# Kernel optimization log

Measured on AMD Instinct MI355X. Metric: run time of the kernel, lower is better.

Reference implementation:

```python
import jax, jax.numpy as jnp
import numpy as np

IN_C, HID_C, OUT_C = 6, 128, 6
B, H, W = 8, 256, 256


def _make_weight(key, oc, ic):
    return jax.random.normal(key, (oc, ic, 5), dtype=jnp.float32) / np.sqrt(ic * 5)


def setup_inputs() -> dict:
    key = jax.random.key(0)
    ks = jax.random.split(key, 5)
    x = jax.random.normal(ks[0], (B, IN_C, H, W), dtype=jnp.float32)
    return {
        "x": x,
        "w1": _make_weight(ks[1], HID_C, IN_C),
        "b1": jnp.zeros((HID_C,), jnp.float32),
        "w2": _make_weight(ks[2], HID_C, HID_C),
        "b2": jnp.zeros((HID_C,), jnp.float32),
        "w3": _make_weight(ks[3], HID_C, HID_C),
        "b3": jnp.zeros((HID_C,), jnp.float32),
        "w4": _make_weight(ks[4], OUT_C, HID_C),
        "b4": jnp.zeros((OUT_C,), jnp.float32),
    }


def cross_conv(x, w, b):
    # w: [oc, ic, 5] -> dense 3x3 kernel with 5-point cross stencil
    oc, ic, _ = w.shape
    k = jnp.zeros((oc, ic, 3, 3), dtype=w.dtype)
    k = k.at[:, :, 1, 1].set(w[:, :, 0])  # center
    k = k.at[:, :, 0, 1].set(w[:, :, 1])  # up
    k = k.at[:, :, 2, 1].set(w[:, :, 2])  # down
    k = k.at[:, :, 1, 0].set(w[:, :, 3])  # left
    k = k.at[:, :, 1, 2].set(w[:, :, 4])  # right
    y = jax.lax.conv_general_dilated(
        x, k, window_strides=(1, 1), padding="SAME",
        dimension_numbers=("NCHW", "OIHW", "NCHW"))
    return y + b[None, :, None, None]


def reference(x, w1, b1, w2, b2, w3, b3, w4, b4):
    h = jax.nn.relu(cross_conv(x, w1, b1))
    h = jax.nn.relu(cross_conv(h, w2, b2))
    h = jax.nn.relu(cross_conv(h, w3, b3))
    return cross_conv(h, w4, b4)
```

## Files before the change

### kernel.cpp

```cpp
#include <hip/hip_runtime.h>


#define BB   8
#define HH   256
#define WW   256

typedef _Float16 f16x8 __attribute__((ext_vector_type(8)));
typedef float    f32x4 __attribute__((ext_vector_type(4)));

__device__ _Float16 W1g[128 * 32];
__device__ _Float16 W2g[20 * 128 * 32];
__device__ _Float16 W3g[20 * 128 * 32];
__device__ _Float16 W4g[5 * 16 * 128];

__global__ void prep(const float* __restrict__ w1, const float* __restrict__ w2,
                     const float* __restrict__ w3, const float* __restrict__ w4)
{
    int idx = blockIdx.x * 256 + threadIdx.x;
    if (idx < 81920) {
        int icb = idx & 31, oc = (idx >> 5) & 127, ks = idx >> 12;
        int tap = ks >> 2, ic = (ks & 3) * 32 + icb;
        W2g[idx] = (_Float16)w2[(oc * 128 + ic) * 5 + tap];
    } else if (idx < 163840) {
        int k = idx - 81920;
        int icb = k & 31, oc = (k >> 5) & 127, ks = k >> 12;
        int tap = ks >> 2, ic = (ks & 3) * 32 + icb;
        W3g[k] = (_Float16)w3[(oc * 128 + ic) * 5 + tap];
    } else if (idx < 174080) {
        int k = idx - 163840;
        int t = k / 2048, oc = (k >> 7) & 15, ic = k & 127;
        W4g[k] = (_Float16)((oc < 6) ? w4[(oc * 128 + ic) * 5 + t] : 0.f);
    } else if (idx < 178176) {
        int k = idx - 174080;
        int kk = k & 31, oc = k >> 5;
        float v = 0.f;
        if (kk < 30) {
            int tap = (kk * 43) >> 8;
            int ic = kk - 6 * tap;
            v = w1[(oc * 6 + ic) * 5 + tap];
        }
        W1g[k] = (_Float16)v;
    }
}

template<int HALF, bool EDGE>
__device__ __forceinline__ void g1_stage(const float* __restrict__ xb,
                                         _Float16* __restrict__ Ap,
                                         int px, int gi0, int gj0)
{
#pragma unroll
    for (int it = 0; it < 15; ++it) {
        const int k = 2 * it + HALF;
        const int tap = k / 6, ic = k - 6 * tap;
        const int DI = (tap == 1) ? -1 : ((tap == 2) ? 1 : 0);
        const int DJ = (tap == 3) ? -1 : ((tap == 4) ? 1 : 0);
        const float* sp = xb + ic * 65536 + DI * 256 + DJ;
        float v;
        if (EDGE) {
            const int gi = gi0 + DI, gj = gj0 + DJ;
            v = ((unsigned)gi < 256u && (unsigned)gj < 256u) ? *sp : 0.f;
        } else {
            v = *sp;
        }
        Ap[px * 40 + k] = (_Float16)v;
    }
    Ap[px * 40 + 30 + HALF] = (_Float16)0.f;
}

__global__ __launch_bounds__(256, 3) void g1(
    const float* __restrict__ x, const float* __restrict__ bias,
    _Float16* __restrict__ outp)
{
    __shared__ _Float16 Ap[128 * 40];
    const int tid = threadIdx.x;
    const int j0 = blockIdx.x * 16, i0 = blockIdx.y * 8, b = blockIdx.z;
    const int px = tid & 127, half = tid >> 7;
    const int pr = px >> 4, pp = px & 15;
    const bool edge = (blockIdx.y == 0) | (blockIdx.y == 31) |
                      (blockIdx.x == 0) | (blockIdx.x == 15);
    const int gi0 = i0 + pr, gj0 = j0 + pp;
    const float* xb = x + (size_t)b * 6 * 65536 + gi0 * 256 + gj0;

    if (edge) {
        if (half == 0) g1_stage<0, true >(xb, Ap, px, gi0, gj0);
        else           g1_stage<1, true >(xb, Ap, px, gi0, gj0);
    } else {
        if (half == 0) g1_stage<0, false>(xb, Ap, px, gi0, gj0);
        else           g1_stage<1, false>(xb, Ap, px, gi0, gj0);
    }
    __syncthreads();

    const int lane = tid & 63, w = tid >> 6, l16 = lane & 15, quad = lane >> 4;
    f32x4 acc[2][8] = {};
    f16x8 a0 = *(const f16x8*)&Ap[((2 * w + 0) * 16 + l16) * 40 + quad * 8];
    f16x8 a1 = *(const f16x8*)&Ap[((2 * w + 1) * 16 + l16) * 40 + quad * 8];
#pragma unroll
    for (int nf = 0; nf < 8; ++nf) {
        f16x8 bf = *(const f16x8*)&W1g[(nf * 16 + l16) * 32 + quad * 8];
        acc[0][nf] = __builtin_amdgcn_mfma_f32_16x16x32_f16(a0, bf, acc[0][nf], 0, 0, 0);
        acc[1][nf] = __builtin_amdgcn_mfma_f32_16x16x32_f16(a1, bf, acc[1][nf], 0, 0, 0);
    }
#pragma unroll
    for (int mf = 0; mf < 2; ++mf) {
        const size_t rowb = ((size_t)b * 256 + i0 + 2 * w + mf) * 256 + j0;
#pragma unroll
        for (int nf = 0; nf < 8; ++nf) {
            const float bv = bias[nf * 16 + l16];
#pragma unroll
            for (int r = 0; r < 4; ++r)
                outp[(rowb + quad * 4 + r) * 128 + nf * 16 + l16] =
                    (_Float16)fmaxf(acc[mf][nf][r] + bv, 0.f);
        }
    }
}

template<int LAYER>
__global__ __launch_bounds__(256, 2) void gmid(
    const _Float16* __restrict__ in, const float* __restrict__ bias,
    _Float16* __restrict__ outp)
{
    const _Float16* wt = (LAYER == 2) ? W2g : W3g;
    __shared__ __align__(16) _Float16 Al[180 * 128];
    const int tid = threadIdx.x;
    const int lane = tid & 63, w = tid >> 6;
    const int j0 = blockIdx.x * 16, i0 = blockIdx.y * 8, b = blockIdx.z;
    const bool top = (blockIdx.y == 0), bot = (blockIdx.y == 31);
    const bool left = (blockIdx.x == 0), right = (blockIdx.x == 15);

    {
        const int pxl = lane & 15;
#pragma unroll
        for (int k = 0; k < 12; ++k) {
            const int m = w + 4 * k;
            if (m < 45) {
                const int s = 4 * m + (lane >> 4);
                const int r = (s * 114) >> 11;
                const int p = s - 18 * r;
                int gi = i0 - 1 + r; gi = gi < 0 ? 0 : (gi > 255 ? 255 : gi);
                int gj = j0 - 1 + p; gj = gj < 0 ? 0 : (gj > 255 ? 255 : gj);
                const _Float16* src = in + (((size_t)(b * 256 + gi)) * 256 + gj) * 128
                                         + ((pxl ^ (s & 7)) << 3);
                __builtin_amdgcn_global_load_lds(
                    (const __attribute__((address_space(1))) void*)src,
                    (__attribute__((address_space(3))) void*)(Al + m * 512),
                    16, 0, 0);
            }
        }
    }
    __syncthreads();
    if (top | bot | left | right) {
#pragma unroll
        for (int pass = 0; pass < 2; ++pass) {
            const int gidx = (tid >> 3) + 32 * pass, c = tid & 7;
            int sid = -1;
            if (gidx < 18)      { if (top)   sid = gidx; }
            else if (gidx < 36) { if (bot)   sid = 162 + gidx - 18; }
            else if (gidx < 46) { if (left)  sid = (gidx - 36) * 18; }
            else if (gidx < 56) { if (right) sid = (gidx - 46) * 18 + 17; }
            if (sid >= 0) {
                const f16x8 z = {};
                *(f16x8*)(Al + sid * 128 + c * 16)     = z;
                *(f16x8*)(Al + sid * 128 + c * 16 + 8) = z;
            }
        }
        __syncthreads();
    }

    const int l16 = lane & 15, quad = lane >> 4;
    const int n0 = w * 32;

    const _Float16* wb = wt + (size_t)(n0 + l16) * 32 + quad * 8;

    f32x4 acc[8][2] = {};
    const int DR[5] = {1, 0, 2, 1, 1}, DP[5] = {1, 1, 1, 0, 2};

    auto lda = [&](int ks, int r) -> f16x8 {
        const int tap = ks >> 2, kc = ks & 3;
        const int s = (DR[tap] + r) * 18 + DP[tap] + l16;
        const int ch = (kc * 4 + quad) ^ (s & 7);
        return *(const f16x8*)&Al[s * 128 + ch * 8];
    };

    f16x8 bc[2], bn[2], ac[8], an[8];
#pragma unroll
    for (int nf = 0; nf < 2; ++nf) bc[nf] = *(const f16x8*)(wb + nf * 512);
#pragma unroll
    for (int r = 0; r < 8; ++r) ac[r] = lda(0, r);

#pragma unroll
    for (int ks = 0; ks < 20; ++ks) {
        if (ks < 19) {
#pragma unroll
            for (int nf = 0; nf < 2; ++nf)
                bn[nf] = *(const f16x8*)(wb + (size_t)(ks + 1) * 4096 + nf * 512);
#pragma unroll
            for (int r = 0; r < 8; ++r) an[r] = lda(ks + 1, r);
        }
        __builtin_amdgcn_s_setprio(1);
#pragma unroll
        for (int r = 0; r < 8; ++r)
#pragma unroll
            for (int nf = 0; nf < 2; ++nf)
                acc[r][nf] = __builtin_amdgcn_mfma_f32_16x16x32_f16(
                    ac[r], bc[nf], acc[r][nf], 0, 0, 0);
        __builtin_amdgcn_s_setprio(0);
#pragma unroll
        for (int nf = 0; nf < 2; ++nf) bc[nf] = bn[nf];
#pragma unroll
        for (int r = 0; r < 8; ++r) ac[r] = an[r];
    }

#pragma unroll
    for (int r = 0; r < 8; ++r) {
        const size_t rowb = ((size_t)b * 256 + i0 + r) * 256 + j0;
#pragma unroll
        for (int nf = 0; nf < 2; ++nf) {
            const float bv = bias[n0 + nf * 16 + l16];
#pragma unroll
            for (int vi = 0; vi < 4; ++vi)
                outp[(rowb + quad * 4 + vi) * 128 + n0 + nf * 16 + l16] =
                    (_Float16)fmaxf(acc[r][nf][vi] + bv, 0.f);
        }
    }
}

__global__ __launch_bounds__(256, 3) void g4(
    const _Float16* __restrict__ in, const float* __restrict__ bias,
    float* __restrict__ outp)
{
    __shared__ __align__(16) _Float16 Al[180 * 128];
    const int tid = threadIdx.x;
    const int lane = tid & 63, w = tid >> 6;
    const int j0 = blockIdx.x * 16, i0 = blockIdx.y * 8, b = blockIdx.z;
    const bool top = (blockIdx.y == 0), bot = (blockIdx.y == 31);
    const bool left = (blockIdx.x == 0), right = (blockIdx.x == 15);

    {
        const int pxl = lane & 15;
#pragma unroll
        for (int k = 0; k < 12; ++k) {
            const int m = w + 4 * k;
            if (m < 45) {
                const int s = 4 * m + (lane >> 4);
                const int r = (s * 114) >> 11;
                const int p = s - 18 * r;
                int gi = i0 - 1 + r; gi = gi < 0 ? 0 : (gi > 255 ? 255 : gi);
                int gj = j0 - 1 + p; gj = gj < 0 ? 0 : (gj > 255 ? 255 : gj);
                const _Float16* src = in + (((size_t)(b * 256 + gi)) * 256 + gj) * 128
                                         + ((pxl ^ (s & 7)) << 3);
                __builtin_amdgcn_global_load_lds(
                    (const __attribute__((address_space(1))) void*)src,
                    (__attribute__((address_space(3))) void*)(Al + m * 512),
                    16, 0, 0);
            }
        }
    }
    __syncthreads();
    if (top | bot | left | right) {
#pragma unroll
        for (int pass = 0; pass < 2; ++pass) {
            const int gidx = (tid >> 3) + 32 * pass, c = tid & 7;
            int sid = -1;
            if (gidx < 18)      { if (top)   sid = gidx; }
            else if (gidx < 36) { if (bot)   sid = 162 + gidx - 18; }
            else if (gidx < 46) { if (left)  sid = (gidx - 36) * 18; }
            else if (gidx < 56) { if (right) sid = (gidx - 46) * 18 + 17; }
            if (sid >= 0) {
                const f16x8 z = {};
                *(f16x8*)(Al + sid * 128 + c * 16)     = z;
                *(f16x8*)(Al + sid * 128 + c * 16 + 8) = z;
            }
        }
        __syncthreads();
    }

    const int l16 = lane & 15, quad = lane >> 4;
    const int DR[5] = {1, 0, 2, 1, 1}, DP[5] = {1, 1, 1, 0, 2};

    auto lda = [&](int ks, int row) -> f16x8 {
        const int tap = ks >> 2, kc = ks & 3;
        const int s = (DR[tap] + row) * 18 + DP[tap] + l16;
        const int ch = (kc * 4 + quad) ^ (s & 7);
        return *(const f16x8*)&Al[s * 128 + ch * 8];
    };
    auto ldb = [&](int ks) -> f16x8 {
        const int tap = ks >> 2, kc = ks & 3;
        return *(const f16x8*)&W4g[(size_t)(tap * 16 + l16) * 128 + kc * 32 + quad * 8];
    };

    f32x4 acc[2] = {};
    f16x8 bfc = ldb(0), bfn;
    f16x8 afc0 = lda(0, 2 * w), afc1 = lda(0, 2 * w + 1), afn0, afn1;
#pragma unroll
    for (int ks = 0; ks < 20; ++ks) {
        if (ks < 19) {
            bfn  = ldb(ks + 1);
            afn0 = lda(ks + 1, 2 * w);
            afn1 = lda(ks + 1, 2 * w + 1);
        }
        __builtin_amdgcn_s_setprio(1);
        acc[0] = __builtin_amdgcn_mfma_f32_16x16x32_f16(afc0, bfc, acc[0], 0, 0, 0);
        acc[1] = __builtin_amdgcn_mfma_f32_16x16x32_f16(afc1, bfc, acc[1], 0, 0, 0);
        __builtin_amdgcn_s_setprio(0);
        bfc = bfn; afc0 = afn0; afc1 = afn1;
    }

    if (l16 < 6) {
        const float bb = bias[l16];
#pragma unroll
        for (int f = 0; f < 2; ++f) {
            const int i = i0 + 2 * w + f;
#pragma unroll
            for (int vi = 0; vi < 4; ++vi) {
                int jj = j0 + quad * 4 + vi;
                outp[(((size_t)b * 6 + l16) << 16) + i * 256 + jj] = acc[f][vi] + bb;
            }
        }
    }
}

extern "C" void kernel_launch(void* const* d_in, const int* in_sizes, int n_in,
                              void* d_out, int out_size, void* d_ws, size_t ws_size,
                              hipStream_t stream) {
    const float* x  = (const float*)d_in[0];
    const float* w1 = (const float*)d_in[1];
    const float* b1 = (const float*)d_in[2];
    const float* w2 = (const float*)d_in[3];
    const float* b2 = (const float*)d_in[4];
    const float* w3 = (const float*)d_in[5];
    const float* b3 = (const float*)d_in[6];
    const float* w4 = (const float*)d_in[7];
    const float* b4 = (const float*)d_in[8];
    float* out = (float*)d_out;

    const size_t act = (size_t)BB * HH * WW * 128;
    _Float16* A1 = (_Float16*)d_ws;
    _Float16* A2 = A1 + act;

    prep<<<696, 256, 0, stream>>>(w1, w2, w3, w4);
    dim3 blk(256, 1, 1);
    dim3 gm(16, 32, 8);
    g1<<<gm, blk, 0, stream>>>(x, b1, A1);
    gmid<2><<<gm, blk, 0, stream>>>(A1, b2, A2);
    gmid<3><<<gm, blk, 0, stream>>>(A2, b3, A1);
    g4<<<gm, blk, 0, stream>>>(A1, b4, out);
}
```

Before: 348.5 us.

## Make mid-layer conv blocks persistent over batch, prefetching next tile during stores

The two hidden-layer conv kernels now launch one block per spatial tile and loop over all 8 batch images inside the block. After the MFMA loop for one image finishes, the block issues the async global-to-LDS loads for the next image before writing the current outputs, so staging overlaps the store epilogue. Weight pointers and bias values are hoisted out of the loop. This cuts block scheduling and tail overhead, but adds intra-block barriers and leaves a single LDS buffer, so overlap is limited.

Measured after the change: 608.5 us. 74.6% more time.

```diff
diff --git a/kernel.cpp b/kernel.cpp
--- a/kernel.cpp
+++ b/kernel.cpp
@@ -123,6 +123,133 @@
     __shared__ __align__(16) _Float16 Al[180 * 128];
     const int tid = threadIdx.x;
     const int lane = tid & 63, w = tid >> 6;
+    const int j0 = blockIdx.x * 16, i0 = blockIdx.y * 8;
+    const bool top = (blockIdx.y == 0), bot = (blockIdx.y == 31);
+    const bool left = (blockIdx.x == 0), right = (blockIdx.x == 15);
+    const bool edge = top | bot | left | right;
+    const int pxl = lane & 15;
+
+    auto stage = [&](int bb) {
+#pragma unroll
+        for (int k = 0; k < 12; ++k) {
+            const int m = w + 4 * k;
+            if (m < 45) {
+                const int s = 4 * m + (lane >> 4);
+                const int r = (s * 114) >> 11;
+                const int p = s - 18 * r;
+                int gi = i0 - 1 + r; gi = gi < 0 ? 0 : (gi > 255 ? 255 : gi);
+                int gj = j0 - 1 + p; gj = gj < 0 ? 0 : (gj > 255 ? 255 : gj);
+                const _Float16* src = in + (((size_t)(bb * 256 + gi)) * 256 + gj) * 128
+                                         + ((pxl ^ (s & 7)) << 3);
+                __builtin_amdgcn_global_load_lds(
+                    (const __attribute__((address_space(1))) void*)src,
+                    (__attribute__((address_space(3))) void*)(Al + m * 512),
+                    16, 0, 0);
+            }
+        }
+    };
+
+    auto fixup = [&]() {
+#pragma unroll
+        for (int pass = 0; pass < 2; ++pass) {
+            const int gidx = (tid >> 3) + 32 * pass, c = tid & 7;
+            int sid = -1;
+            if (gidx < 18)      { if (top)   sid = gidx; }
+            else if (gidx < 36) { if (bot)   sid = 162 + gidx - 18; }
+            else if (gidx < 46) { if (left)  sid = (gidx - 36) * 18; }
+            else if (gidx < 56) { if (right) sid = (gidx - 46) * 18 + 17; }
+            if (sid >= 0) {
+                const f16x8 z = {};
+                *(f16x8*)(Al + sid * 128 + c * 16)     = z;
+                *(f16x8*)(Al + sid * 128 + c * 16 + 8) = z;
+            }
+        }
+    };
+
+    const int l16 = lane & 15, quad = lane >> 4;
+    const int n0 = w * 32;
+    const _Float16* wb = wt + (size_t)(n0 + l16) * 32 + quad * 8;
+    const int DR[5] = {1, 0, 2, 1, 1}, DP[5] = {1, 1, 1, 0, 2};
+    const float bv0 = bias[n0 + l16], bv1 = bias[n0 + 16 + l16];
+
+    auto lda = [&](int ks, int r) -> f16x8 {
+        const int tap = ks >> 2, kc = ks & 3;
+        const int s = (DR[tap] + r) * 18 + DP[tap] + l16;
+        const int ch = (kc * 4 + quad) ^ (s & 7);
+        return *(const f16x8*)&Al[s * 128 + ch * 8];
+    };
+
+    stage(0);
+    __syncthreads();
+    if (edge) { fixup(); __syncthreads(); }
+
+#pragma unroll 1
+    for (int t = 0; t < 8; ++t) {
+        f32x4 acc[8][2] = {};
+        f16x8 bc[2], bn[2], ac[8], an[8];
+#pragma unroll
+        for (int nf = 0; nf < 2; ++nf) bc[nf] = *(const f16x8*)(wb + nf * 512);
+#pragma unroll
+        for (int r = 0; r < 8; ++r) ac[r] = lda(0, r);
+
+#pragma unroll
+        for (int ks = 0; ks < 20; ++ks) {
+            if (ks < 19) {
+#pragma unroll
+                for (int nf = 0; nf < 2; ++nf)
+                    bn[nf] = *(const f16x8*)(wb + (size_t)(ks + 1) * 4096 + nf * 512);
+#pragma unroll
+                for (int r = 0; r < 8; ++r) an[r] = lda(ks + 1, r);
+            }
+            __builtin_amdgcn_s_setprio(1);
+#pragma unroll
+            for (int r = 0; r < 8; ++r)
+#pragma unroll
+                for (int nf = 0; nf < 2; ++nf)
+                    acc[r][nf] = __builtin_amdgcn_mfma_f32_16x16x32_f16(
+                        ac[r], bc[nf], acc[r][nf], 0, 0, 0);
+            __builtin_amdgcn_s_setprio(0);
+#pragma unroll
+            for (int nf = 0; nf < 2; ++nf) bc[nf] = bn[nf];
+#pragma unroll
+            for (int r = 0; r < 8; ++r) ac[r] = an[r];
+        }
+
+        if (t < 7) {
+            asm volatile("s_waitcnt lgkmcnt(0)" ::: "memory");
+            __builtin_amdgcn_sched_barrier(0);
+            __builtin_amdgcn_s_barrier();
+            stage(t + 1);
+        }
+
+#pragma unroll
+        for (int r = 0; r < 8; ++r) {
+            const size_t rowb = ((size_t)t * 256 + i0 + r) * 256 + j0;
+#pragma unroll
+            for (int vi = 0; vi < 4; ++vi) {
+                outp[(rowb + quad * 4 + vi) * 128 + n0 + l16] =
+                    (_Float16)fmaxf(acc[r][0][vi] + bv0, 0.f);
+                outp[(rowb + quad * 4 + vi) * 128 + n0 + 16 + l16] =
+                    (_Float16)fmaxf(acc[r][1][vi] + bv1, 0.f);
+            }
+        }
+
+        if (t < 7) {
+            asm volatile("s_waitcnt vmcnt(0)" ::: "memory");
+            __builtin_amdgcn_sched_barrier(0);
+            __builtin_amdgcn_s_barrier();
+            if (edge) { fixup(); __syncthreads(); }
+        }
+    }
+}
+
+__global__ __launch_bounds__(256, 3) void g4(
+    const _Float16* __restrict__ in, const float* __restrict__ bias,
+    float* __restrict__ outp)
+{
+    __shared__ __align__(16) _Float16 Al[180 * 128];
+    const int tid = threadIdx.x;
+    const int lane = tid & 63, w = tid >> 6;
     const int j0 = blockIdx.x * 16, i0 = blockIdx.y * 8, b = blockIdx.z;
     const bool top = (blockIdx.y == 0), bot = (blockIdx.y == 31);
     const bool left = (blockIdx.x == 0), right = (blockIdx.x == 15);
@@ -167,114 +294,6 @@
     }
 
     const int l16 = lane & 15, quad = lane >> 4;
-    const int n0 = w * 32;
-
-    const _Float16* wb = wt + (size_t)(n0 + l16) * 32 + quad * 8;
-
-    f32x4 acc[8][2] = {};
-    const int DR[5] = {1, 0, 2, 1, 1}, DP[5] = {1, 1, 1, 0, 2};
-
-    auto lda = [&](int ks, int r) -> f16x8 {
-        const int tap = ks >> 2, kc = ks & 3;
-        const int s = (DR[tap] + r) * 18 + DP[tap] + l16;
-        const int ch = (kc * 4 + quad) ^ (s & 7);
-        return *(const f16x8*)&Al[s * 128 + ch * 8];
-    };
-
-    f16x8 bc[2], bn[2], ac[8], an[8];
-#pragma unroll
-    for (int nf = 0; nf < 2; ++nf) bc[nf] = *(const f16x8*)(wb + nf * 512);
-#pragma unroll
-    for (int r = 0; r < 8; ++r) ac[r] = lda(0, r);
-
-#pragma unroll
-    for (int ks = 0; ks < 20; ++ks) {
-        if (ks < 19) {
-#pragma unroll
-            for (int nf = 0; nf < 2; ++nf)
-                bn[nf] = *(const f16x8*)(wb + (size_t)(ks + 1) * 4096 + nf * 512);
-#pragma unroll
-            for (int r = 0; r < 8; ++r) an[r] = lda(ks + 1, r);
-        }
-        __builtin_amdgcn_s_setprio(1);
-#pragma unroll
-        for (int r = 0; r < 8; ++r)
-#pragma unroll
-            for (int nf = 0; nf < 2; ++nf)
-                acc[r][nf] = __builtin_amdgcn_mfma_f32_16x16x32_f16(
-                    ac[r], bc[nf], acc[r][nf], 0, 0, 0);
-        __builtin_amdgcn_s_setprio(0);
-#pragma unroll
-        for (int nf = 0; nf < 2; ++nf) bc[nf] = bn[nf];
-#pragma unroll
-        for (int r = 0; r < 8; ++r) ac[r] = an[r];
-    }
-
-#pragma unroll
-    for (int r = 0; r < 8; ++r) {
-        const size_t rowb = ((size_t)b * 256 + i0 + r) * 256 + j0;
-#pragma unroll
-        for (int nf = 0; nf < 2; ++nf) {
-            const float bv = bias[n0 + nf * 16 + l16];
-#pragma unroll
-            for (int vi = 0; vi < 4; ++vi)
-                outp[(rowb + quad * 4 + vi) * 128 + n0 + nf * 16 + l16] =
-                    (_Float16)fmaxf(acc[r][nf][vi] + bv, 0.f);
-        }
-    }
-}
-
-__global__ __launch_bounds__(256, 3) void g4(
-    const _Float16* __restrict__ in, const float* __restrict__ bias,
-    float* __restrict__ outp)
-{
-    __shared__ __align__(16) _Float16 Al[180 * 128];
-    const int tid = threadIdx.x;
-    const int lane = tid & 63, w = tid >> 6;
-    const int j0 = blockIdx.x * 16, i0 = blockIdx.y * 8, b = blockIdx.z;
-    const bool top = (blockIdx.y == 0), bot = (blockIdx.y == 31);
-    const bool left = (blockIdx.x == 0), right = (blockIdx.x == 15);
-
-    {
-        const int pxl = lane & 15;
-#pragma unroll
-        for (int k = 0; k < 12; ++k) {
-            const int m = w + 4 * k;
-            if (m < 45) {
-                const int s = 4 * m + (lane >> 4);
-                const int r = (s * 114) >> 11;
-                const int p = s - 18 * r;
-                int gi = i0 - 1 + r; gi = gi < 0 ? 0 : (gi > 255 ? 255 : gi);
-                int gj = j0 - 1 + p; gj = gj < 0 ? 0 : (gj > 255 ? 255 : gj);
-                const _Float16* src = in + (((size_t)(b * 256 + gi)) * 256 + gj) * 128
-                                         + ((pxl ^ (s & 7)) << 3);
-                __builtin_amdgcn_global_load_lds(
-                    (const __attribute__((address_space(1))) void*)src,
-                    (__attribute__((address_space(3))) void*)(Al + m * 512),
-                    16, 0, 0);
-            }
-        }
-    }
-    __syncthreads();
-    if (top | bot | left | right) {
-#pragma unroll
-        for (int pass = 0; pass < 2; ++pass) {
-            const int gidx = (tid >> 3) + 32 * pass, c = tid & 7;
-            int sid = -1;
-            if (gidx < 18)      { if (top)   sid = gidx; }
-            else if (gidx < 36) { if (bot)   sid = 162 + gidx - 18; }
-            else if (gidx < 46) { if (left)  sid = (gidx - 36) * 18; }
-            else if (gidx < 56) { if (right) sid = (gidx - 46) * 18 + 17; }
-            if (sid >= 0) {
-                const f16x8 z = {};
-                *(f16x8*)(Al + sid * 128 + c * 16)     = z;
-                *(f16x8*)(Al + sid * 128 + c * 16 + 8) = z;
-            }
-        }
-        __syncthreads();
-    }
-
-    const int l16 = lane & 15, quad = lane >> 4;
     const int DR[5] = {1, 0, 2, 1, 1}, DP[5] = {1, 1, 1, 0, 2};
 
     auto lda = [&](int ks, int row) -> f16x8 {
@@ -341,7 +360,7 @@
     dim3 blk(256, 1, 1);
     dim3 gm(16, 32, 8);
     g1<<<gm, blk, 0, stream>>>(x, b1, A1);
-    gmid<2><<<gm, blk, 0, stream>>>(A1, b2, A2);
-    gmid<3><<<gm, blk, 0, stream>>>(A2, b3, A1);
+    gmid<2><<<dim3(16, 32, 1), blk, 0, stream>>>(A1, b2, A2);
+    gmid<3><<<dim3(16, 32, 1), blk, 0, stream>>>(A2, b3, A1);
     g4<<<gm, blk, 0, stream>>>(A1, b4, out);
 }
```

## Pre-convert input to NHWC fp16 and load layer-1 MFMA operands directly

Applied to the files above, without the earlier changes.

Adds a prepx kernel that transposes the fp32 NCHW input into an 8-channel-padded fp16 NHWC buffer, placed in the second activation workspace. Layer 1 then loads each tap's 8 channels as a single 16-byte vector straight into MFMA A fragments, doing two K=32 MFMAs per output tile. This replaces the shared-memory staging of 30 scalar strided loads and the block barrier. The cost is an extra kernel launch and a full pass over the input, plus padded work: the 5 taps are spread over 64 K slots instead of 30.

Result: no change. 354.6 us (+1.8%).

```diff
diff --git a/kernel.cpp b/kernel.cpp
--- a/kernel.cpp
+++ b/kernel.cpp
@@ -8,7 +8,7 @@
 typedef _Float16 f16x8 __attribute__((ext_vector_type(8)));
 typedef float    f32x4 __attribute__((ext_vector_type(4)));
 
-__device__ _Float16 W1g[128 * 32];
+__device__ _Float16 W1g2[128 * 64];
 __device__ _Float16 W2g[20 * 128 * 32];
 __device__ _Float16 W3g[20 * 128 * 32];
 __device__ _Float16 W4g[5 * 16 * 128];
@@ -30,76 +30,67 @@
         int k = idx - 163840;
         int t = k / 2048, oc = (k >> 7) & 15, ic = k & 127;
         W4g[k] = (_Float16)((oc < 6) ? w4[(oc * 128 + ic) * 5 + t] : 0.f);
-    } else if (idx < 178176) {
+    } else if (idx < 182272) {
         int k = idx - 174080;
-        int kk = k & 31, oc = k >> 5;
-        float v = 0.f;
-        if (kk < 30) {
-            int tap = (kk * 43) >> 8;
-            int ic = kk - 6 * tap;
-            v = w1[(oc * 6 + ic) * 5 + tap];
-        }
-        W1g[k] = (_Float16)v;
-    }
-}
-
-template<int HALF, bool EDGE>
-__device__ __forceinline__ void g1_stage(const float* __restrict__ xb,
-                                         _Float16* __restrict__ Ap,
-                                         int px, int gi0, int gj0)
-{
-#pragma unroll
-    for (int it = 0; it < 15; ++it) {
-        const int k = 2 * it + HALF;
-        const int tap = k / 6, ic = k - 6 * tap;
-        const int DI = (tap == 1) ? -1 : ((tap == 2) ? 1 : 0);
-        const int DJ = (tap == 3) ? -1 : ((tap == 4) ? 1 : 0);
-        const float* sp = xb + ic * 65536 + DI * 256 + DJ;
-        float v;
-        if (EDGE) {
-            const int gi = gi0 + DI, gj = gj0 + DJ;
-            v = ((unsigned)gi < 256u && (unsigned)gj < 256u) ? *sp : 0.f;
-        } else {
-            v = *sp;
-        }
-        Ap[px * 40 + k] = (_Float16)v;
-    }
-    Ap[px * 40 + 30 + HALF] = (_Float16)0.f;
+        int oc = k >> 6, kk = k & 63;
+        int tap = kk >> 3, ic = kk & 7;
+        float v = (tap < 5 && ic < 6) ? w1[(oc * 6 + ic) * 5 + tap] : 0.f;
+        W1g2[k] = (_Float16)v;
+    }
+}
+
+__global__ void prepx(const float* __restrict__ x, _Float16* __restrict__ xh)
+{
+    int idx = blockIdx.x * 256 + threadIdx.x;
+    int c = idx & 7, pix = idx >> 3;
+    float v = 0.f;
+    if (c < 6) {
+        int b = pix >> 16, ij = pix & 65535;
+        v = x[((size_t)(b * 6 + c) << 16) + ij];
+    }
+    xh[idx] = (_Float16)v;
 }
 
 __global__ __launch_bounds__(256, 3) void g1(
-    const float* __restrict__ x, const float* __restrict__ bias,
+    const _Float16* __restrict__ xh, const float* __restrict__ bias,
     _Float16* __restrict__ outp)
 {
-    __shared__ _Float16 Ap[128 * 40];
     const int tid = threadIdx.x;
+    const int lane = tid & 63, w = tid >> 6, l16 = lane & 15, quad = lane >> 4;
     const int j0 = blockIdx.x * 16, i0 = blockIdx.y * 8, b = blockIdx.z;
-    const int px = tid & 127, half = tid >> 7;
-    const int pr = px >> 4, pp = px & 15;
     const bool edge = (blockIdx.y == 0) | (blockIdx.y == 31) |
                       (blockIdx.x == 0) | (blockIdx.x == 15);
-    const int gi0 = i0 + pr, gj0 = j0 + pp;
-    const float* xb = x + (size_t)b * 6 * 65536 + gi0 * 256 + gj0;
-
-    if (edge) {
-        if (half == 0) g1_stage<0, true >(xb, Ap, px, gi0, gj0);
-        else           g1_stage<1, true >(xb, Ap, px, gi0, gj0);
-    } else {
-        if (half == 0) g1_stage<0, false>(xb, Ap, px, gi0, gj0);
-        else           g1_stage<1, false>(xb, Ap, px, gi0, gj0);
-    }
-    __syncthreads();
-
-    const int lane = tid & 63, w = tid >> 6, l16 = lane & 15, quad = lane >> 4;
+
+    const int di0 = (quad == 1) ? -1 : ((quad == 2) ? 1 : 0);
+    const int dj0 = (quad == 3) ? -1 : 0;
+
+    f16x8 a[2][2];
+#pragma unroll
+    for (int mf = 0; mf < 2; ++mf) {
+        const int gi = i0 + 2 * w + mf, gj = j0 + l16;
+#pragma unroll
+        for (int kh = 0; kh < 2; ++kh) {
+            const int gia = kh ? gi : gi + di0;
+            const int gja = kh ? gj + 1 : gj + dj0;
+            if (edge && !(((unsigned)gia < 256u) && ((unsigned)gja < 256u))) {
+                a[mf][kh] = (f16x8){0, 0, 0, 0, 0, 0, 0, 0};
+            } else {
+                a[mf][kh] = *(const f16x8*)&xh[(((size_t)b * 256 + gia) * 256 + gja) * 8];
+            }
+        }
+    }
+
     f32x4 acc[2][8] = {};
-    f16x8 a0 = *(const f16x8*)&Ap[((2 * w + 0) * 16 + l16) * 40 + quad * 8];
-    f16x8 a1 = *(const f16x8*)&Ap[((2 * w + 1) * 16 + l16) * 40 + quad * 8];
 #pragma unroll
     for (int nf = 0; nf < 8; ++nf) {
-        f16x8 bf = *(const f16x8*)&W1g[(nf * 16 + l16) * 32 + quad * 8];
-        acc[0][nf] = __builtin_amdgcn_mfma_f32_16x16x32_f16(a0, bf, acc[0][nf], 0, 0, 0);
-        acc[1][nf] = __builtin_amdgcn_mfma_f32_16x16x32_f16(a1, bf, acc[1][nf], 0, 0, 0);
-    }
+        const f16x8 b0 = *(const f16x8*)&W1g2[(nf * 16 + l16) * 64 + quad * 8];
+        const f16x8 b1 = *(const f16x8*)&W1g2[(nf * 16 + l16) * 64 + 32 + quad * 8];
+        acc[0][nf] = __builtin_amdgcn_mfma_f32_16x16x32_f16(a[0][0], b0, acc[0][nf], 0, 0, 0);
+        acc[0][nf] = __builtin_amdgcn_mfma_f32_16x16x32_f16(a[0][1], b1, acc[0][nf], 0, 0, 0);
+        acc[1][nf] = __builtin_amdgcn_mfma_f32_16x16x32_f16(a[1][0], b0, acc[1][nf], 0, 0, 0);
+        acc[1][nf] = __builtin_amdgcn_mfma_f32_16x16x32_f16(a[1][1], b1, acc[1][nf], 0, 0, 0);
+    }
+
 #pragma unroll
     for (int mf = 0; mf < 2; ++mf) {
         const size_t rowb = ((size_t)b * 256 + i0 + 2 * w + mf) * 256 + j0;
@@ -336,11 +327,13 @@
     const size_t act = (size_t)BB * HH * WW * 128;
     _Float16* A1 = (_Float16*)d_ws;
     _Float16* A2 = A1 + act;
-
-    prep<<<696, 256, 0, stream>>>(w1, w2, w3, w4);
+    _Float16* xh = A2;
+
+    prep<<<712, 256, 0, stream>>>(w1, w2, w3, w4);
+    prepx<<<16384, 256, 0, stream>>>(x, xh);
     dim3 blk(256, 1, 1);
     dim3 gm(16, 32, 8);
-    g1<<<gm, blk, 0, stream>>>(x, b1, A1);
+    g1<<<gm, blk, 0, stream>>>(xh, b1, A1);
     gmid<2><<<gm, blk, 0, stream>>>(A1, b2, A2);
     gmid<3><<<gm, blk, 0, stream>>>(A2, b3, A1);
     g4<<<gm, blk, 0, stream>>>(A1, b4, out);
```
